# Performance work log

Hardware: AMD Instinct MI355X
Metric: run time of the kernel (lower is better)

Reference implementation:

```python
import jax, jax.numpy as jnp
import numpy as np

B, C, H, W = 4, 512, 64, 64
C8 = C // 8


def setup_inputs() -> dict:
    key = jax.random.key(0)
    ks = jax.random.split(key, 8)
    return {
        "x": jax.random.normal(ks[0], (B, C, H, W), jnp.float32),
        "wb": jax.random.normal(ks[1], (C8, C), jnp.float32) * 0.05,
        "bb": jax.random.normal(ks[2], (C8,), jnp.float32) * 0.05,
        "wc": jax.random.normal(ks[3], (C8, C), jnp.float32) * 0.05,
        "bc": jax.random.normal(ks[4], (C8,), jnp.float32) * 0.05,
        "wd": jax.random.normal(ks[5], (C, C), jnp.float32) * 0.05,
        "bd": jax.random.normal(ks[6], (C,), jnp.float32) * 0.05,
        "alpha": jax.random.normal(ks[7], (1,), jnp.float32),
    }


def reference(x, wb, bb, wc, bc, wd, bd, alpha):
    b, c, h, w = x.shape
    n = h * w
    xf = x.reshape(b, c, n)  # [B, C, N]
    # 1x1 convs == per-pixel channel matmuls
    feat_b = jnp.einsum('kc,bcn->bkn', wb, xf) + bb[:, None]  # [B, C/8, N]
    feat_c = jnp.einsum('kc,bcn->bkn', wc, xf) + bc[:, None]  # [B, C/8, N]
    # attention_s[n, m] = softmax_m( feat_b[:, n] . feat_c[:, m] )  (no scaling, as in source)
    scores = jnp.einsum('bkn,bkm->bnm', feat_b, feat_c)  # [B, N, N]
    attn = jax.nn.softmax(scores, axis=-1)
    feat_d = jnp.einsum('oc,bcn->bon', wd, xf) + bd[:, None]  # [B, C, N]
    # feat_e = bmm(feat_d, attn^T): fe[c, n] = sum_m fd[c, m] * attn[n, m]
    feat_e = jnp.einsum('bcm,bnm->bcn', feat_d, attn).reshape(b, c, h, w)
    return alpha[0] * feat_e + x
```

## Files before the change

### kernel.cpp

```cpp
#include <hip/hip_runtime.h>
#include <hip/hip_bf16.h>

#define NB 4
#define CC 512
#define CK 64
#define NN 4096

typedef unsigned short u16;
typedef __attribute__((ext_vector_type(8))) __bf16 bf16x8;
typedef __attribute__((ext_vector_type(4))) float f32x4;
typedef __attribute__((ext_vector_type(4))) unsigned int u32x4;
typedef __attribute__((ext_vector_type(8))) unsigned short u16x8;
typedef __attribute__((ext_vector_type(4))) unsigned short u16x4;

__device__ __forceinline__ u16 f2b(float f) {
  union { float f; unsigned u; } x; x.f = f;
  unsigned r = x.u + 0x7fffu + ((x.u >> 16) & 1u);
  return (u16)(r >> 16);
}
__device__ __forceinline__ float b2f(u16 u) {
  union { unsigned u; float f; } x; x.u = ((unsigned)u) << 16; return x.f;
}
__device__ __forceinline__ u16 cvt_bf16(float f) {
  union { __bf16 h; u16 u; } c; c.h = (__bf16)f; return c.u;
}
__device__ __forceinline__ float fast_exp2(float x) {
  float r;
  asm("v_exp_f32 %0, %1" : "=v"(r) : "v"(x));
  return r;
}
__device__ __forceinline__ void lds_barrier() {
  asm volatile("s_waitcnt lgkmcnt(0)" ::: "memory");
  __builtin_amdgcn_s_barrier();
}

#define MFMA16(a, b, c) __builtin_amdgcn_mfma_f32_16x16x32_bf16((a), (b), (c), 0, 0, 0)

__global__ __launch_bounds__(256) void proj_qk(
    const float* __restrict__ x,
    const float* __restrict__ wb, const float* __restrict__ bb,
    const float* __restrict__ wc, const float* __restrict__ bc,
    u16* __restrict__ Qhi, u16* __restrict__ Qlo,
    u16* __restrict__ Khi, u16* __restrict__ Klo)
{
  const int tid = threadIdx.x;
  const int n0 = blockIdx.x * 64;
  const int which = blockIdx.y;
  const int b = blockIdx.z;
  const float* w   = which ? wc : wb;
  const float* bia = which ? bc : bb;
  u16* oh = which ? Khi : Qhi;
  u16* ol = which ? Klo : Qlo;
  const float qsc = which ? 1.0f : 1.44269504088896340736f;

  __shared__ u16 Wh[64][40], Wl[64][40], Xh[64][40], Xl[64][40];

  const int lane = tid & 63, wid = tid >> 6;
  const int wr = wid >> 1, wn = wid & 1;
  const int l15 = lane & 15, lk = (lane >> 4) * 8;

  f32x4 acc[2][2] = {};

  for (int kk = 0; kk < CC; kk += 32) {
    {
      const int row = tid >> 2, c0 = (tid & 3) * 8;
      const float* src = w + (size_t)row * CC + kk + c0;
#pragma unroll
      for (int i = 0; i < 8; ++i) {
        float v = src[i];
        u16 h = f2b(v);
        Wh[row][c0 + i] = h;
        Wl[row][c0 + i] = f2b(v - b2f(h));
      }
    }
    {
      const int cc2 = tid >> 3, j0 = (tid & 7) * 8;
      const float* src = x + ((size_t)b * CC + kk + cc2) * NN + n0 + j0;
#pragma unroll
      for (int i = 0; i < 8; ++i) {
        float v = src[i];
        u16 h = f2b(v);
        Xh[j0 + i][cc2] = h;
        Xl[j0 + i][cc2] = f2b(v - b2f(h));
      }
    }
    __syncthreads();
#pragma unroll
    for (int fi = 0; fi < 2; ++fi) {
      const int ar = wr * 32 + fi * 16 + l15;
      bf16x8 ah = *(const bf16x8*)&Wh[ar][lk];
      bf16x8 al = *(const bf16x8*)&Wl[ar][lk];
#pragma unroll
      for (int fj = 0; fj < 2; ++fj) {
        const int br = wn * 32 + fj * 16 + l15;
        bf16x8 bh = *(const bf16x8*)&Xh[br][lk];
        bf16x8 bl = *(const bf16x8*)&Xl[br][lk];
        acc[fi][fj] = MFMA16(ah, bh, acc[fi][fj]);
        acc[fi][fj] = MFMA16(ah, bl, acc[fi][fj]);
        acc[fi][fj] = MFMA16(al, bh, acc[fi][fj]);
      }
    }
    __syncthreads();
  }

#pragma unroll
  for (int fi = 0; fi < 2; ++fi) {
    const int d0 = wr * 32 + fi * 16 + (lane >> 4) * 4;
#pragma unroll
    for (int fj = 0; fj < 2; ++fj) {
      const int n = n0 + wn * 32 + fj * 16 + l15;
      u16x4 vh, vl;
#pragma unroll
      for (int r = 0; r < 4; ++r) {
        float v = (acc[fi][fj][r] + bia[d0 + r]) * qsc;
        u16 h = f2b(v);
        vh[r] = h;
        vl[r] = f2b(v - b2f(h));
      }
      *(u16x4*)&oh[((size_t)b * NN + n) * CK + d0] = vh;
      *(u16x4*)&ol[((size_t)b * NN + n) * CK + d0] = vl;
    }
  }
}

__global__ __launch_bounds__(256) void proj_v(
    const float* __restrict__ x,
    const float* __restrict__ wd, const float* __restrict__ bd,
    u16* __restrict__ Vt)
{
  const int tid = threadIdx.x;
  const int n0 = blockIdx.x * 64;
  const int o0 = blockIdx.y * 64;
  const int b = blockIdx.z;

  __shared__ u16 Wt[64][40], Xt[64][40];
  const int lane = tid & 63, wid = tid >> 6;
  const int wr = wid >> 1, wn = wid & 1;
  const int l15 = lane & 15, lk = (lane >> 4) * 8;

  f32x4 acc[2][2] = {};
  for (int kk = 0; kk < CC; kk += 32) {
    {
      const int row = tid >> 2, c0 = (tid & 3) * 8;
      const float* src = wd + (size_t)(o0 + row) * CC + kk + c0;
#pragma unroll
      for (int i = 0; i < 8; ++i) Wt[row][c0 + i] = f2b(src[i]);
    }
    {
      const int cc2 = tid >> 3, j0 = (tid & 7) * 8;
      const float* src = x + ((size_t)b * CC + kk + cc2) * NN + n0 + j0;
#pragma unroll
      for (int i = 0; i < 8; ++i) Xt[j0 + i][cc2] = f2b(src[i]);
    }
    __syncthreads();
#pragma unroll
    for (int fi = 0; fi < 2; ++fi) {
      bf16x8 a = *(const bf16x8*)&Wt[wr * 32 + fi * 16 + l15][lk];
#pragma unroll
      for (int fj = 0; fj < 2; ++fj) {
        bf16x8 bv = *(const bf16x8*)&Xt[wn * 32 + fj * 16 + l15][lk];
        acc[fi][fj] = MFMA16(a, bv, acc[fi][fj]);
      }
    }
    __syncthreads();
  }
#pragma unroll
  for (int fi = 0; fi < 2; ++fi) {
    const int d0 = o0 + wr * 32 + fi * 16 + (lane >> 4) * 4;
#pragma unroll
    for (int fj = 0; fj < 2; ++fj) {
      const int n = n0 + wn * 32 + fj * 16 + l15;
#pragma unroll
      for (int r = 0; r < 4; ++r)
        Vt[((size_t)b * CC + d0 + r) * NN + n] = f2b(acc[fi][fj][r] + bd[d0 + r]);
    }
  }
}

struct alignas(16) AttnLds {
  u16 kh[64][64];
  u16 kl[64][64];
  float s[64][68];
  u16 p[64][64];
  float m[64];
  float l[64];
  float sc[64];
};

__global__ __launch_bounds__(256, 2) void attn(
    const u16* __restrict__ Qhi, const u16* __restrict__ Qlo,
    const u16* __restrict__ Khi, const u16* __restrict__ Klo,
    const u16* __restrict__ Vt,
    const float* __restrict__ x, const float* __restrict__ alpha,
    float* __restrict__ out)
{
  __shared__ AttnLds L;
  const int tid = threadIdx.x;
  const int lane = tid & 63, wid = tid >> 6;
  const int bid = blockIdx.x;
  const int b = (bid >> 1) & 3;
  const int qt = bid >> 3;
  const int ohalf = bid & 1;
  const int q0 = qt * 64;
  const int l15 = lane & 15;
  const int lk8 = (lane >> 4) * 8;

  const int srow = tid >> 2;
  const int sch  = (tid & 3) * 16;
  const int ssw0 = sch ^ ((srow & 7) << 3);
  const int ssw1 = (sch + 8) ^ ((srow & 7) << 3);

  bf16x8 qah[2], qal[2];
  {
    const size_t qg = ((size_t)b * NN + q0 + wid * 16 + l15) * CK + lk8;
    qah[0] = *(const bf16x8*)&Qhi[qg];
    qah[1] = *(const bf16x8*)&Qhi[qg + 32];
    qal[0] = *(const bf16x8*)&Qlo[qg];
    qal[1] = *(const bf16x8*)&Qlo[qg + 32];
  }
  {
    const size_t g = ((size_t)b * NN + srow) * CK + sch;
    *(u32x4*)&L.kh[srow][ssw0] = *(const u32x4*)&Khi[g];
    *(u32x4*)&L.kh[srow][ssw1] = *(const u32x4*)&Khi[g + 8];
    *(u32x4*)&L.kl[srow][ssw0] = *(const u32x4*)&Klo[g];
    *(u32x4*)&L.kl[srow][ssw1] = *(const u32x4*)&Klo[g + 8];
  }
  if (tid < 64) { L.m[tid] = -__builtin_huge_valf(); L.l[tid] = 0.f; }

  const u16* vbase = Vt + ((size_t)b * CC + ohalf * 256 + wid * 64 + l15) * NN + lk8;

  f32x4 accO[4][4] = {};

  __syncthreads();

  for (int t = 0; t < 64; ++t) {
    const int m0 = t * 64;
    const bool hasNext = (t < 63);

    u32x4 kh0, kh1, kl0, kl1;
    if (hasNext) {
      const size_t g = ((size_t)b * NN + m0 + 64 + srow) * CK + sch;
      kh0 = *(const u32x4*)&Khi[g];
      kh1 = *(const u32x4*)&Khi[g + 8];
      kl0 = *(const u32x4*)&Klo[g];
      kl1 = *(const u32x4*)&Klo[g + 8];
    }
    bf16x8 vr[2][4];
#pragma unroll
    for (int f_ = 0; f_ < 4; ++f_)
#pragma unroll
      for (int ks = 0; ks < 2; ++ks)
        vr[ks][f_] = *(const bf16x8*)(vbase + (size_t)f_ * 16 * NN + m0 + ks * 32);

    __builtin_amdgcn_s_setprio(1);
#pragma unroll
    for (int fj = 0; fj < 4; ++fj) {
      f32x4 s = {};
#pragma unroll
      for (int ks = 0; ks < 2; ++ks) {
        const int k = ks * 32 + lk8;
        const int br = fj * 16 + l15;
        bf16x8 bh = *(const bf16x8*)&L.kh[br][k ^ ((br & 7) << 3)];
        bf16x8 bl = *(const bf16x8*)&L.kl[br][k ^ ((br & 7) << 3)];
        s = MFMA16(qah[ks], bh, s);
        s = MFMA16(qah[ks], bl, s);
        s = MFMA16(qal[ks], bh, s);
      }
      const int r0 = wid * 16 + (lane >> 4) * 4, c0 = fj * 16 + l15;
#pragma unroll
      for (int r = 0; r < 4; ++r) L.s[r0 + r][c0] = s[r];
    }
    __builtin_amdgcn_s_setprio(0);
    lds_barrier();

    if (hasNext) {
      *(u32x4*)&L.kh[srow][ssw0] = kh0;
      *(u32x4*)&L.kh[srow][ssw1] = kh1;
      *(u32x4*)&L.kl[srow][ssw0] = kl0;
      *(u32x4*)&L.kl[srow][ssw1] = kl1;
    }
    {
      const int row = srow, sub = tid & 3;
      const float* sr = &L.s[row][sch];
      f32x4 a0 = *(const f32x4*)&sr[0];
      f32x4 a1 = *(const f32x4*)&sr[4];
      f32x4 a2 = *(const f32x4*)&sr[8];
      f32x4 a3 = *(const f32x4*)&sr[12];
      float mx = fmaxf(fmaxf(fmaxf(a0[0], a0[1]), fmaxf(a0[2], a0[3])),
                       fmaxf(fmaxf(a1[0], a1[1]), fmaxf(a1[2], a1[3])));
      mx = fmaxf(mx, fmaxf(fmaxf(fmaxf(a2[0], a2[1]), fmaxf(a2[2], a2[3])),
                           fmaxf(fmaxf(a3[0], a3[1]), fmaxf(a3[2], a3[3]))));
      mx = fmaxf(mx, __shfl_xor(mx, 1));
      mx = fmaxf(mx, __shfl_xor(mx, 2));
      const float mOld = L.m[row];
      const bool grow = (mx > mOld + 11.5f);
      const float mNew = grow ? mx : mOld;
      float pv[16];
      float sum = 0.f;
#pragma unroll
      for (int j = 0; j < 4; ++j) { pv[j]      = fast_exp2(a0[j] - mNew); sum += pv[j]; }
#pragma unroll
      for (int j = 0; j < 4; ++j) { pv[4 + j]  = fast_exp2(a1[j] - mNew); sum += pv[4 + j]; }
#pragma unroll
      for (int j = 0; j < 4; ++j) { pv[8 + j]  = fast_exp2(a2[j] - mNew); sum += pv[8 + j]; }
#pragma unroll
      for (int j = 0; j < 4; ++j) { pv[12 + j] = fast_exp2(a3[j] - mNew); sum += pv[12 + j]; }
      sum += __shfl_xor(sum, 1);
      sum += __shfl_xor(sum, 2);
      const float scf = grow ? fast_exp2(mOld - mNew) : 1.0f;
      if (sub == 0) {
        if (grow) L.m[row] = mNew;
        L.l[row] = L.l[row] * scf + sum;
        L.sc[row] = scf;
      }
      u16x8 pb0, pb1;
#pragma unroll
      for (int j = 0; j < 8; ++j) pb0[j] = cvt_bf16(pv[j]);
#pragma unroll
      for (int j = 0; j < 8; ++j) pb1[j] = cvt_bf16(pv[8 + j]);
      *(u16x8*)&L.p[row][ssw0] = pb0;
      *(u16x8*)&L.p[row][ssw1] = pb1;
    }
    lds_barrier();

    {
      f32x4 scv[4];
      bool need = false;
#pragma unroll
      for (int f_ = 0; f_ < 4; ++f_) {
        scv[f_] = *(const f32x4*)&L.sc[f_ * 16 + (lane >> 4) * 4];
        need |= (scv[f_][0] != 1.0f) | (scv[f_][1] != 1.0f) |
                (scv[f_][2] != 1.0f) | (scv[f_][3] != 1.0f);
      }
      if (__any(need)) {
#pragma unroll
        for (int f_ = 0; f_ < 4; ++f_)
#pragma unroll
          for (int fj = 0; fj < 4; ++fj)
#pragma unroll
            for (int r = 0; r < 4; ++r)
              accO[f_][fj][r] *= scv[f_][r];
      }
    }
    __builtin_amdgcn_s_setprio(1);
#pragma unroll
    for (int ks = 0; ks < 2; ++ks) {
      const int k = ks * 32 + lk8;
      bf16x8 a[4];
#pragma unroll
      for (int f_ = 0; f_ < 4; ++f_) {
        const int ar = f_ * 16 + l15;
        a[f_] = *(const bf16x8*)&L.p[ar][k ^ ((ar & 7) << 3)];
      }
#pragma unroll
      for (int fj = 0; fj < 4; ++fj)
#pragma unroll
        for (int f_ = 0; f_ < 4; ++f_)
          accO[f_][fj] = MFMA16(a[f_], vr[ks][fj], accO[f_][fj]);
    }
    __builtin_amdgcn_s_setprio(0);
  }
  __syncthreads();
  const float al = alpha[0];
#pragma unroll
  for (int f_ = 0; f_ < 4; ++f_) {
    const int r0 = f_ * 16 + (lane >> 4) * 4;
    const float rl0 = 1.f / L.l[r0],     rl1 = 1.f / L.l[r0 + 1];
    const float rl2 = 1.f / L.l[r0 + 2], rl3 = 1.f / L.l[r0 + 3];
    const int n_ = q0 + r0;
#pragma unroll
    for (int fj = 0; fj < 4; ++fj) {
      const int c_ = ohalf * 256 + wid * 64 + fj * 16 + l15;
      const size_t g = ((size_t)b * CC + c_) * NN + n_;
      f32x4 xv = *(const f32x4*)&x[g];
      f32x4 ov;
      ov[0] = fmaf(al, accO[f_][fj][0] * rl0, xv[0]);
      ov[1] = fmaf(al, accO[f_][fj][1] * rl1, xv[1]);
      ov[2] = fmaf(al, accO[f_][fj][2] * rl2, xv[2]);
      ov[3] = fmaf(al, accO[f_][fj][3] * rl3, xv[3]);
      *(f32x4*)&out[g] = ov;
    }
  }
}

extern "C" void kernel_launch(void* const* d_in, const int* in_sizes, int n_in,
                              void* d_out, int out_size, void* d_ws, size_t ws_size,
                              hipStream_t stream) {
  const float* x     = (const float*)d_in[0];
  const float* wb    = (const float*)d_in[1];
  const float* bb    = (const float*)d_in[2];
  const float* wc    = (const float*)d_in[3];
  const float* bc    = (const float*)d_in[4];
  const float* wd    = (const float*)d_in[5];
  const float* bd    = (const float*)d_in[6];
  const float* alpha = (const float*)d_in[7];
  float* out = (float*)d_out;

  u16* Qhi = (u16*)d_ws;
  u16* Qlo = Qhi + (size_t)NB * NN * CK;
  u16* Khi = Qlo + (size_t)NB * NN * CK;
  u16* Klo = Khi + (size_t)NB * NN * CK;
  u16* Vt  = Klo + (size_t)NB * NN * CK;

  proj_qk<<<dim3(NN / 64, 2, NB), 256, 0, stream>>>(x, wb, bb, wc, bc, Qhi, Qlo, Khi, Klo);
  proj_v<<<dim3(NN / 64, CC / 64, NB), 256, 0, stream>>>(x, wd, bd, Vt);
  attn<<<dim3(512), 256, 0, stream>>>(Qhi, Qlo, Khi, Klo, Vt, x, alpha, out);
}
```

Baseline: 231.5 us.

## Enlarge proj_v tiles to 128x128, vectorize loads, use hardware bf16 conversion

The V projection kernel moves from 64x64 to 128x128 output tiles per block, with each wave computing a 4x4 grid of MFMA fragments and reusing B fragments held in registers. This raises data reuse and cuts redundant loads of x and wd. Global loads in both projection kernels become float4 vector loads, and the manual round-to-nearest bf16 conversion is replaced by the native bf16 cast. The larger tiles use more registers and LDS and launch fewer blocks, which may lower occupancy. The projections are also a small share of the total time next to the attention kernel.

```diff
diff --git a/kernel.cpp b/kernel.cpp
--- a/kernel.cpp
+++ b/kernel.cpp
@@ -13,11 +13,6 @@
 typedef __attribute__((ext_vector_type(8))) unsigned short u16x8;
 typedef __attribute__((ext_vector_type(4))) unsigned short u16x4;
 
-__device__ __forceinline__ u16 f2b(float f) {
-  union { float f; unsigned u; } x; x.f = f;
-  unsigned r = x.u + 0x7fffu + ((x.u >> 16) & 1u);
-  return (u16)(r >> 16);
-}
 __device__ __forceinline__ float b2f(u16 u) {
   union { unsigned u; float f; } x; x.u = ((unsigned)u) << 16; return x.f;
 }
@@ -64,24 +59,33 @@
   for (int kk = 0; kk < CC; kk += 32) {
     {
       const int row = tid >> 2, c0 = (tid & 3) * 8;
-      const float* src = w + (size_t)row * CC + kk + c0;
-#pragma unroll
-      for (int i = 0; i < 8; ++i) {
-        float v = src[i];
-        u16 h = f2b(v);
-        Wh[row][c0 + i] = h;
-        Wl[row][c0 + i] = f2b(v - b2f(h));
-      }
+      const f32x4* src = (const f32x4*)(w + (size_t)row * CC + kk + c0);
+      u16x8 hh, ll;
+#pragma unroll
+      for (int i = 0; i < 2; ++i) {
+        f32x4 v = src[i];
+#pragma unroll
+        for (int r = 0; r < 4; ++r) {
+          u16 h = cvt_bf16(v[r]);
+          hh[i * 4 + r] = h;
+          ll[i * 4 + r] = cvt_bf16(v[r] - b2f(h));
+        }
+      }
+      *(u16x8*)&Wh[row][c0] = hh;
+      *(u16x8*)&Wl[row][c0] = ll;
     }
     {
       const int cc2 = tid >> 3, j0 = (tid & 7) * 8;
-      const float* src = x + ((size_t)b * CC + kk + cc2) * NN + n0 + j0;
-#pragma unroll
-      for (int i = 0; i < 8; ++i) {
-        float v = src[i];
-        u16 h = f2b(v);
-        Xh[j0 + i][cc2] = h;
-        Xl[j0 + i][cc2] = f2b(v - b2f(h));
+      const f32x4* src = (const f32x4*)(x + ((size_t)b * CC + kk + cc2) * NN + n0 + j0);
+#pragma unroll
+      for (int i = 0; i < 2; ++i) {
+        f32x4 v = src[i];
+#pragma unroll
+        for (int r = 0; r < 4; ++r) {
+          u16 h = cvt_bf16(v[r]);
+          Xh[j0 + i * 4 + r][cc2] = h;
+          Xl[j0 + i * 4 + r][cc2] = cvt_bf16(v[r] - b2f(h));
+        }
       }
     }
     __syncthreads();
@@ -113,9 +117,9 @@
 #pragma unroll
       for (int r = 0; r < 4; ++r) {
         float v = (acc[fi][fj][r] + bia[d0 + r]) * qsc;
-        u16 h = f2b(v);
+        u16 h = cvt_bf16(v);
         vh[r] = h;
-        vl[r] = f2b(v - b2f(h));
+        vl[r] = cvt_bf16(v - b2f(h));
       }
       *(u16x4*)&oh[((size_t)b * NN + n) * CK + d0] = vh;
       *(u16x4*)&ol[((size_t)b * NN + n) * CK + d0] = vl;
@@ -129,50 +133,62 @@
     u16* __restrict__ Vt)
 {
   const int tid = threadIdx.x;
-  const int n0 = blockIdx.x * 64;
-  const int o0 = blockIdx.y * 64;
+  const int n0 = blockIdx.x * 128;
+  const int o0 = blockIdx.y * 128;
   const int b = blockIdx.z;
 
-  __shared__ u16 Wt[64][40], Xt[64][40];
+  __shared__ u16 Wt[128][40], Xt[128][40];
   const int lane = tid & 63, wid = tid >> 6;
   const int wr = wid >> 1, wn = wid & 1;
   const int l15 = lane & 15, lk = (lane >> 4) * 8;
 
-  f32x4 acc[2][2] = {};
+  f32x4 acc[4][4] = {};
   for (int kk = 0; kk < CC; kk += 32) {
     {
-      const int row = tid >> 2, c0 = (tid & 3) * 8;
-      const float* src = wd + (size_t)(o0 + row) * CC + kk + c0;
-#pragma unroll
-      for (int i = 0; i < 8; ++i) Wt[row][c0 + i] = f2b(src[i]);
-    }
-    {
-      const int cc2 = tid >> 3, j0 = (tid & 7) * 8;
-      const float* src = x + ((size_t)b * CC + kk + cc2) * NN + n0 + j0;
-#pragma unroll
-      for (int i = 0; i < 8; ++i) Xt[j0 + i][cc2] = f2b(src[i]);
+      const int row = tid >> 1, c0 = (tid & 1) * 16;
+      const f32x4* src = (const f32x4*)(wd + (size_t)(o0 + row) * CC + kk + c0);
+#pragma unroll
+      for (int i = 0; i < 4; ++i) {
+        f32x4 v = src[i];
+        u16x4 p;
+#pragma unroll
+        for (int r = 0; r < 4; ++r) p[r] = cvt_bf16(v[r]);
+        *(u16x4*)&Wt[row][c0 + i * 4] = p;
+      }
+    }
+    {
+      const int cc2 = tid >> 3, j0 = (tid & 7) * 16;
+      const f32x4* src = (const f32x4*)(x + ((size_t)b * CC + kk + cc2) * NN + n0 + j0);
+#pragma unroll
+      for (int i = 0; i < 4; ++i) {
+        f32x4 v = src[i];
+#pragma unroll
+        for (int r = 0; r < 4; ++r) Xt[j0 + i * 4 + r][cc2] = cvt_bf16(v[r]);
+      }
     }
     __syncthreads();
-#pragma unroll
-    for (int fi = 0; fi < 2; ++fi) {
-      bf16x8 a = *(const bf16x8*)&Wt[wr * 32 + fi * 16 + l15][lk];
-#pragma unroll
-      for (int fj = 0; fj < 2; ++fj) {
-        bf16x8 bv = *(const bf16x8*)&Xt[wn * 32 + fj * 16 + l15][lk];
-        acc[fi][fj] = MFMA16(a, bv, acc[fi][fj]);
-      }
+    bf16x8 bvv[4];
+#pragma unroll
+    for (int fj = 0; fj < 4; ++fj)
+      bvv[fj] = *(const bf16x8*)&Xt[wn * 64 + fj * 16 + l15][lk];
+#pragma unroll
+    for (int fi = 0; fi < 4; ++fi) {
+      bf16x8 a = *(const bf16x8*)&Wt[wr * 64 + fi * 16 + l15][lk];
+#pragma unroll
+      for (int fj = 0; fj < 4; ++fj)
+        acc[fi][fj] = MFMA16(a, bvv[fj], acc[fi][fj]);
     }
     __syncthreads();
   }
 #pragma unroll
-  for (int fi = 0; fi < 2; ++fi) {
-    const int d0 = o0 + wr * 32 + fi * 16 + (lane >> 4) * 4;
-#pragma unroll
-    for (int fj = 0; fj < 2; ++fj) {
-      const int n = n0 + wn * 32 + fj * 16 + l15;
+  for (int fi = 0; fi < 4; ++fi) {
+    const int d0 = o0 + wr * 64 + fi * 16 + (lane >> 4) * 4;
+#pragma unroll
+    for (int fj = 0; fj < 4; ++fj) {
+      const int n = n0 + wn * 64 + fj * 16 + l15;
 #pragma unroll
       for (int r = 0; r < 4; ++r)
-        Vt[((size_t)b * CC + d0 + r) * NN + n] = f2b(acc[fi][fj][r] + bd[d0 + r]);
+        Vt[((size_t)b * CC + d0 + r) * NN + n] = cvt_bf16(acc[fi][fj][r] + bd[d0 + r]);
     }
   }
 }
@@ -403,6 +419,6 @@
   u16* Vt  = Klo + (size_t)NB * NN * CK;
 
   proj_qk<<<dim3(NN / 64, 2, NB), 256, 0, stream>>>(x, wb, bb, wc, bc, Qhi, Qlo, Khi, Klo);
-  proj_v<<<dim3(NN / 64, CC / 64, NB), 256, 0, stream>>>(x, wd, bd, Vt);
+  proj_v<<<dim3(NN / 128, CC / 128, NB), 256, 0, stream>>>(x, wd, bd, Vt);
   attn<<<dim3(512), 256, 0, stream>>>(Qhi, Qlo, Khi, Klo, Vt, x, alpha, out);
 }
```

New measurement: 216.0 us. 6.7% less time.
